# Kernel tuning notes

Hardware: AMD Instinct MI355X
Metric: run time of the kernel (lower is better)

Reference implementation:

```python
import jax, jax.numpy as jnp
import numpy as np

B, L, D = 2, 1024, 2048
E, K = 8, 2
H, HS = 1408, 2816


def setup_inputs() -> dict:
    key = jax.random.key(0)
    ks = jax.random.split(key, 9)
    s = 0.02  # param init scale
    return {
        "x": jax.random.normal(ks[0], (B, L, D), dtype=jnp.float32),
        "gate_w": jax.random.normal(ks[1], (E, D), dtype=jnp.float32) * s,
        "w_gate": jax.random.normal(ks[2], (E, D, H), dtype=jnp.float32) * s,
        "w_up": jax.random.normal(ks[3], (E, D, H), dtype=jnp.float32) * s,
        "w_down": jax.random.normal(ks[4], (E, H, D), dtype=jnp.float32) * s,
        "shgate_w": jax.random.normal(ks[5], (D,), dtype=jnp.float32) * s,
        "shw_gate": jax.random.normal(ks[6], (D, HS), dtype=jnp.float32) * s,
        "shw_up": jax.random.normal(ks[7], (D, HS), dtype=jnp.float32) * s,
        "shw_down": jax.random.normal(ks[8], (HS, D), dtype=jnp.float32) * s,
    }


def reference(x, gate_w, w_gate, w_up, w_down, shgate_w, shw_gate, shw_up, shw_down):
    b, l, d = x.shape
    xf = x.reshape(-1, d)  # [T, D]

    # --- router: softmax over expert logits, top-k, renormalize ---
    logits = jnp.einsum("td,ed->te", xf.astype(jnp.float32), gate_w)
    probs = jax.nn.softmax(logits.astype(jnp.float32), axis=-1)  # [T, E]
    weights, indices = jax.lax.top_k(probs, K)                   # [T, K]
    weights = (weights / weights.sum(-1, keepdims=True)).astype(x.dtype)

    # per-token combine weight for each expert: sum of top-k weights routed to e
    onehot = jax.nn.one_hot(indices, E, dtype=x.dtype)           # [T, K, E]
    combine = jnp.einsum("tk,tke->te", weights, onehot)          # [T, E]

    # --- experts (dense vectorized equivalent of masked gather/scatter loop) ---
    g = jnp.einsum("td,edh->teh", xf, w_gate)
    u = jnp.einsum("td,edh->teh", xf, w_up)
    h = jax.nn.silu(g) * u                                       # [T, E, H]
    # fused down-proj + weighted combine; accumulate in fp32 like the original
    out = jnp.einsum("teh,ehd,te->td", h.astype(jnp.float32),
                     w_down.astype(jnp.float32), combine.astype(jnp.float32))

    # --- shared expert with sigmoid gate ---
    sgate = jax.nn.sigmoid(xf @ shgate_w)[:, None]               # [T, 1]
    sh = (jax.nn.silu(xf @ shw_gate) * (xf @ shw_up)) @ shw_down  # [T, D]
    out = out + (sgate * sh).astype(jnp.float32)

    return out.astype(x.dtype).reshape(b, l, d)
```

## Files before the change

### kernel.cpp

```cpp
#include <hip/hip_runtime.h>
#include <hip/hip_bf16.h>
#include <math.h>

#define T_TOK 2048
#define Dd    2048
#define Ee    8
#define Hh    1408
#define HSs   2816
#define CAP   1024

typedef __attribute__((ext_vector_type(8))) __bf16 bf16x8;
typedef __attribute__((ext_vector_type(4))) __bf16 bf16x4;
typedef __attribute__((ext_vector_type(2))) __bf16 bf16x2;
typedef __attribute__((ext_vector_type(4))) float  f32x4;

#define MFMA(a, b, c) __builtin_amdgcn_mfma_f32_16x16x32_bf16(a, b, c, 0, 0, 0)

__device__ __forceinline__ void async_copy16(const __bf16* g, __bf16* l) {
    __builtin_amdgcn_global_load_lds(
        (const __attribute__((address_space(1))) unsigned int*)g,
        (__attribute__((address_space(3))) unsigned int*)l, 16, 0, 0);
}

__global__ void init_cnt(int* __restrict__ cnt) {
    if (threadIdx.x < Ee) cnt[threadIdx.x] = 0;
}

__global__ __launch_bounds__(256) void router_kernel(
    const float* __restrict__ x, const float* __restrict__ gate_w,
    const float* __restrict__ shgate_w,
    int* __restrict__ cnt, int* __restrict__ ptok, int* __restrict__ pslot,
    float* __restrict__ pw, float* __restrict__ sgate)
{
    const int t = blockIdx.x;
    const int tid = threadIdx.x;
    const float* xt = x + (size_t)t * Dd;

    float acc[Ee];
#pragma unroll
    for (int e = 0; e < Ee; e++) acc[e] = 0.f;
    float accs = 0.f;

    for (int d = tid; d < Dd; d += 256) {
        float xv = xt[d];
#pragma unroll
        for (int e = 0; e < Ee; e++) acc[e] += xv * gate_w[e * Dd + d];
        accs += xv * shgate_w[d];
    }

    __shared__ float red[Ee + 1][256];
#pragma unroll
    for (int e = 0; e < Ee; e++) red[e][tid] = acc[e];
    red[Ee][tid] = accs;
    __syncthreads();

    for (int s = 128; s > 0; s >>= 1) {
        if (tid < s) {
#pragma unroll
            for (int e = 0; e <= Ee; e++) red[e][tid] += red[e][tid + s];
        }
        __syncthreads();
    }

    if (tid == 0) {
        float l0 = -1e30f, l1 = -1e30f;
        int i0 = 0, i1 = 0;
#pragma unroll
        for (int e = 0; e < Ee; e++) {
            float v = red[e][0];
            if (v > l0) { l1 = l0; i1 = i0; l0 = v; i0 = e; }
            else if (v > l1) { l1 = v; i1 = e; }
        }
        float w0 = 1.f / (1.f + expf(l1 - l0));
        float w1 = 1.f - w0;

        int p0 = atomicAdd(&cnt[i0], 1);
        if (p0 < CAP) {
            ptok[i0 * CAP + p0] = t; pslot[i0 * CAP + p0] = 2 * t;
            pw[i0 * CAP + p0] = w0;
        }
        int p1 = atomicAdd(&cnt[i1], 1);
        if (p1 < CAP) {
            ptok[i1 * CAP + p1] = t; pslot[i1 * CAP + p1] = 2 * t + 1;
            pw[i1 * CAP + p1] = w1;
        }
        sgate[t] = 1.f / (1.f + expf(-red[Ee][0]));
    }
}

__global__ __launch_bounds__(256) void cvt_x(const float* __restrict__ src,
                                             __bf16* __restrict__ dst)
{
    int i = blockIdx.x * 256 + threadIdx.x;
    float4 v = ((const float4*)src)[i];
    bf16x4 o = { (__bf16)v.x, (__bf16)v.y, (__bf16)v.z, (__bf16)v.w };
    ((bf16x4*)dst)[i] = o;
}

__global__ __launch_bounds__(256) void transpose_cvt(
    const float* __restrict__ src, __bf16* __restrict__ dst, int R, int C)
{
    src += (size_t)blockIdx.z * R * C;
    dst += (size_t)blockIdx.z * R * C;
    __shared__ float tile[64][65];
    const int tid = threadIdx.x, tx = tid & 63, ty = tid >> 6;
    const int c0 = blockIdx.x * 64, r0 = blockIdx.y * 64;
#pragma unroll
    for (int j = 0; j < 16; j++) {
        int r = j * 4 + ty;
        tile[r][tx] = src[(size_t)(r0 + r) * C + c0 + tx];
    }
    __syncthreads();
    const int rp = (tid & 31) * 2;
    const int cg = tid >> 5;
#pragma unroll
    for (int j = 0; j < 8; j++) {
        int c = j * 8 + cg;
        bf16x2 v = { (__bf16)tile[rp][c], (__bf16)tile[rp + 1][c] };
        *(bf16x2*)&dst[(size_t)(c0 + c) * R + r0 + rp] = v;
    }
}

__global__ __launch_bounds__(256, 3) void gateup_all(
    const __bf16* __restrict__ xb,
    const __bf16* __restrict__ wgT, const __bf16* __restrict__ wuT,
    const __bf16* __restrict__ shwgT, const __bf16* __restrict__ shwuT,
    const int* __restrict__ cnt, const int* __restrict__ ptok,
    __bf16* __restrict__ hq, __bf16* __restrict__ shh)
{
    const int bx = blockIdx.x;
    const int tid = threadIdx.x, lane = tid & 63, wave = tid >> 6;
    const int wr = wave >> 1, wc = wave & 1;
    const int lm = lane & 15, lq = lane >> 4;

    bool sh;
    int m0, h0, n, e = 0;
    const __bf16 *bg_mat, *bu_mat;
    if (bx < 1408) {
        sh = false;
        int mtg = bx / 22, ht = bx - mtg * 22;
        e = mtg >> 3; m0 = (mtg & 7) * 128; h0 = ht * 64;
        n = cnt[e]; if (n > CAP) n = CAP;
        if (m0 >= n) return;
        bg_mat = wgT + (size_t)e * Hh * Dd;
        bu_mat = wuT + (size_t)e * Hh * Dd;
    } else {
        sh = true;
        int s = bx - 1408;
        int mt = s / 44, ht = s - mt * 44;
        m0 = mt * 128; h0 = ht * 64; n = T_TOK;
        bg_mat = shwgT; bu_mat = shwuT;
    }

    __shared__ __align__(16) __bf16 stage[8192];
    __shared__ int tok_s[128];

    if (tid < 128) {
        int i = m0 + tid;
        if (sh) tok_s[tid] = i;
        else { int ic = i < n ? i : n - 1; tok_s[tid] = ptok[e * CAP + ic]; }
    }
    __syncthreads();

    const __bf16* pa0 = xb + (size_t)tok_s[wave * 16 + lm] * Dd + lq * 8;
    const __bf16* pa1 = xb + (size_t)tok_s[64 + wave * 16 + lm] * Dd + lq * 8;
    const __bf16* pbg = bg_mat + (size_t)(h0 + wave * 16 + lm) * Dd + lq * 8;
    const __bf16* pbu = bu_mat + (size_t)(h0 + wave * 16 + lm) * Dd + lq * 8;
    __bf16* la0 = stage + wave * 512 + lane * 8;
    __bf16* la1 = stage + (4 + wave) * 512 + lane * 8;
    __bf16* lbg = stage + 4096 + wave * 512 + lane * 8;
    __bf16* lbu = stage + 6144 + wave * 512 + lane * 8;

    f32x4 acc[4][4] = {};

    for (int k0 = 0; k0 < Dd; k0 += 32) {
        async_copy16(pa0, la0); async_copy16(pa1, la1);
        async_copy16(pbg, lbg); async_copy16(pbu, lbu);
        pa0 += 32; pa1 += 32; pbg += 32; pbu += 32;
        __syncthreads();
        bf16x8 af[4], bfr[4];
        const __bf16* bbase = stage + (wc ? 6144 : 4096);
#pragma unroll
        for (int i = 0; i < 4; i++)
            af[i] = *(const bf16x8*)(stage + (wr * 4 + i) * 512 + lane * 8);
#pragma unroll
        for (int j = 0; j < 4; j++)
            bfr[j] = *(const bf16x8*)(bbase + j * 512 + lane * 8);
#pragma unroll
        for (int i = 0; i < 4; i++)
#pragma unroll
            for (int j = 0; j < 4; j++)
                acc[i][j] = MFMA(af[i], bfr[j], acc[i][j]);
        __syncthreads();
    }

    if (wc == 1) {
#pragma unroll
        for (int i = 0; i < 4; i++)
#pragma unroll
            for (int j = 0; j < 4; j++) {
                bf16x4 uv;
#pragma unroll
                for (int r = 0; r < 4; r++) uv[r] = (__bf16)acc[i][j][r];
                *(bf16x4*)(stage + ((wr * 4 + i) * 4 + j) * 256 + lane * 4) = uv;
            }
    }
    __syncthreads();
    if (wc == 0) {
#pragma unroll
        for (int i = 0; i < 4; i++)
#pragma unroll
            for (int j = 0; j < 4; j++) {
                bf16x4 uv = *(const bf16x4*)(stage + ((wr * 4 + i) * 4 + j) * 256 + lane * 4);
                int col = h0 + j * 16 + lm;
#pragma unroll
                for (int r = 0; r < 4; r++) {
                    int grow = m0 + wr * 64 + i * 16 + lq * 4 + r;
                    if (!sh && grow >= n) continue;
                    float g = acc[i][j][r], u = (float)uv[r];
                    float hv = g / (1.f + __expf(-g)) * u;
                    if (sh) shh[(size_t)grow * HSs + col] = (__bf16)hv;
                    else    hq[((size_t)e * CAP + grow) * Hh + col] = (__bf16)hv;
                }
            }
    }
}

__global__ __launch_bounds__(256, 3) void down_all(
    const __bf16* __restrict__ hq, const __bf16* __restrict__ wdT,
    const __bf16* __restrict__ shh, const __bf16* __restrict__ shwdT,
    const int* __restrict__ cnt, const int* __restrict__ pslot,
    const float* __restrict__ pw, const float* __restrict__ sgate,
    float* __restrict__ eo, float* __restrict__ out)
{
    const int bx = blockIdx.x;
    const int tid = threadIdx.x, lane = tid & 63, wave = tid >> 6;
    const int wr = wave >> 1, wc = wave & 1;
    const int lm = lane & 15, lq = lane >> 4;

    bool sh;
    int m0, n0, n, e = 0, kdim;
    if (bx < 1024) {
        sh = false;
        e = bx >> 7; m0 = ((bx >> 4) & 7) * 128; n0 = (bx & 15) * 128;
        n = cnt[e]; if (n > CAP) n = CAP;
        if (m0 >= n) return;
        kdim = Hh;
    } else {
        sh = true;
        int s = bx - 1024;
        m0 = (s >> 4) * 128; n0 = (s & 15) * 128; n = T_TOK;
        kdim = HSs;
    }

    __shared__ __align__(16) __bf16 stage[8192];
    __shared__ int   slot_s[128];
    __shared__ float w_s[128];

    if (!sh && tid < 128) {
        int i = m0 + tid; int ic = i < n ? i : n - 1;
        slot_s[tid] = pslot[e * CAP + ic];
        w_s[tid] = (i < n) ? pw[e * CAP + ic] : 0.f;
    }

    int ar0 = m0 + wave * 16 + lm, ar1 = m0 + 64 + wave * 16 + lm;
    const __bf16 *pa0, *pa1, *pb0, *pb1;
    if (sh) {
        pa0 = shh + (size_t)ar0 * HSs + lq * 8;
        pa1 = shh + (size_t)ar1 * HSs + lq * 8;
        pb0 = shwdT + (size_t)(n0 + wave * 16 + lm) * HSs + lq * 8;
        pb1 = shwdT + (size_t)(n0 + 64 + wave * 16 + lm) * HSs + lq * 8;
    } else {
        int a0c = ar0 < n ? ar0 : n - 1;
        int a1c = ar1 < n ? ar1 : n - 1;
        pa0 = hq + ((size_t)e * CAP + a0c) * Hh + lq * 8;
        pa1 = hq + ((size_t)e * CAP + a1c) * Hh + lq * 8;
        pb0 = wdT + ((size_t)e * Dd + n0 + wave * 16 + lm) * Hh + lq * 8;
        pb1 = wdT + ((size_t)e * Dd + n0 + 64 + wave * 16 + lm) * Hh + lq * 8;
    }
    __bf16* la0 = stage + wave * 512 + lane * 8;
    __bf16* la1 = stage + (4 + wave) * 512 + lane * 8;
    __bf16* lb0 = stage + 4096 + wave * 512 + lane * 8;
    __bf16* lb1 = stage + 4096 + (4 + wave) * 512 + lane * 8;

    f32x4 acc[4][4] = {};

    for (int k0 = 0; k0 < kdim; k0 += 32) {
        async_copy16(pa0, la0); async_copy16(pa1, la1);
        async_copy16(pb0, lb0); async_copy16(pb1, lb1);
        pa0 += 32; pa1 += 32; pb0 += 32; pb1 += 32;
        __syncthreads();
        bf16x8 af[4], bfr[4];
#pragma unroll
        for (int i = 0; i < 4; i++)
            af[i] = *(const bf16x8*)(stage + (wr * 4 + i) * 512 + lane * 8);
#pragma unroll
        for (int j = 0; j < 4; j++)
            bfr[j] = *(const bf16x8*)(stage + 4096 + (wc * 4 + j) * 512 + lane * 8);
#pragma unroll
        for (int i = 0; i < 4; i++)
#pragma unroll
            for (int j = 0; j < 4; j++)
                acc[i][j] = MFMA(af[i], bfr[j], acc[i][j]);
        __syncthreads();
    }

#pragma unroll
    for (int i = 0; i < 4; i++)
#pragma unroll
        for (int r = 0; r < 4; r++) {
            int rloc = wr * 64 + i * 16 + lq * 4 + r;
            if (sh) {
                int t = m0 + rloc;
                float sg = sgate[t];
#pragma unroll
                for (int j = 0; j < 4; j++)
                    out[(size_t)t * Dd + n0 + (wc * 4 + j) * 16 + lm] = sg * acc[i][j][r];
            } else if (m0 + rloc < n) {
                int   slot = slot_s[rloc];
                float w    = w_s[rloc];
#pragma unroll
                for (int j = 0; j < 4; j++)
                    eo[(size_t)slot * Dd + n0 + (wc * 4 + j) * 16 + lm] = w * acc[i][j][r];
            }
        }
}

__global__ __launch_bounds__(256) void combine_kernel(
    const float* __restrict__ eo, float* __restrict__ out)
{
    int i4 = blockIdx.x * 256 + threadIdx.x;
    int t = i4 >> 9;
    int c = i4 & 511;
    float4 o = ((const float4*)out)[i4];
    float4 a = ((const float4*)(eo + (size_t)(2 * t) * Dd))[c];
    float4 b = ((const float4*)(eo + (size_t)(2 * t + 1) * Dd))[c];
    o.x += a.x + b.x; o.y += a.y + b.y; o.z += a.z + b.z; o.w += a.w + b.w;
    ((float4*)out)[i4] = o;
}

extern "C" void kernel_launch(void* const* d_in, const int* in_sizes, int n_in,
                              void* d_out, int out_size, void* d_ws, size_t ws_size,
                              hipStream_t stream) {
    const float* x        = (const float*)d_in[0];
    const float* gate_w   = (const float*)d_in[1];
    const float* w_gate   = (const float*)d_in[2];
    const float* w_up     = (const float*)d_in[3];
    const float* w_down   = (const float*)d_in[4];
    const float* shgate_w = (const float*)d_in[5];
    const float* shw_gate = (const float*)d_in[6];
    const float* shw_up   = (const float*)d_in[7];
    const float* shw_down = (const float*)d_in[8];
    float* out = (float*)d_out;

    char* ws = (char*)d_ws;
    size_t off = 0;
    auto alloc = [&](size_t bytes) { char* p = ws + off; off = (off + bytes + 255) & ~(size_t)255; return p; };
    int*    cnt    = (int*)   alloc(Ee * 4);
    int*    ptok   = (int*)   alloc(Ee * CAP * 4);
    int*    pslot  = (int*)   alloc(Ee * CAP * 4);
    float*  pw     = (float*) alloc(Ee * CAP * 4);
    float*  sgate  = (float*) alloc(T_TOK * 4);
    __bf16* xb     = (__bf16*)alloc((size_t)T_TOK * Dd * 2);
    __bf16* wgT    = (__bf16*)alloc((size_t)Ee * Hh * Dd * 2);
    __bf16* wuT    = (__bf16*)alloc((size_t)Ee * Hh * Dd * 2);
    __bf16* wdT    = (__bf16*)alloc((size_t)Ee * Dd * Hh * 2);
    __bf16* shwgT  = (__bf16*)alloc((size_t)HSs * Dd * 2);
    __bf16* shwuT  = (__bf16*)alloc((size_t)HSs * Dd * 2);
    __bf16* shwdT  = (__bf16*)alloc((size_t)Dd * HSs * 2);
    __bf16* hq     = (__bf16*)alloc((size_t)Ee * CAP * Hh * 2);
    __bf16* shh    = (__bf16*)alloc((size_t)T_TOK * HSs * 2);
    float*  eo     = (float*) alloc((size_t)T_TOK * 2 * Dd * 4);

    dim3 b256(256);

    init_cnt<<<dim3(1), dim3(64), 0, stream>>>(cnt);
    router_kernel<<<dim3(T_TOK), b256, 0, stream>>>(
        x, gate_w, shgate_w, cnt, ptok, pslot, pw, sgate);
    cvt_x<<<dim3(T_TOK * Dd / 4 / 256), b256, 0, stream>>>(x, xb);
    transpose_cvt<<<dim3(Hh / 64, Dd / 64, Ee), b256, 0, stream>>>(w_gate, wgT, Dd, Hh);
    transpose_cvt<<<dim3(Hh / 64, Dd / 64, Ee), b256, 0, stream>>>(w_up, wuT, Dd, Hh);
    transpose_cvt<<<dim3(Dd / 64, Hh / 64, Ee), b256, 0, stream>>>(w_down, wdT, Hh, Dd);
    transpose_cvt<<<dim3(HSs / 64, Dd / 64, 1), b256, 0, stream>>>(shw_gate, shwgT, Dd, HSs);
    transpose_cvt<<<dim3(HSs / 64, Dd / 64, 1), b256, 0, stream>>>(shw_up, shwuT, Dd, HSs);
    transpose_cvt<<<dim3(Dd / 64, HSs / 64, 1), b256, 0, stream>>>(shw_down, shwdT, HSs, Dd);

    gateup_all<<<dim3(1408 + 704), b256, 0, stream>>>(
        xb, wgT, wuT, shwgT, shwuT, cnt, ptok, hq, shh);
    down_all<<<dim3(1024 + 256), b256, 0, stream>>>(
        hq, wdT, shh, shwdT, cnt, pslot, pw, sgate, eo, out);
    combine_kernel<<<dim3(T_TOK * Dd / 4 / 256), b256, 0, stream>>>(eo, out);
}
```

Measured before the change: 811.7 us.

## Enlarge GEMM tiles in gate/up and down kernels for more reuse per load

The gate/up kernel now computes a 128x128 output tile, with each wave holding both gate and up accumulators. This removes the LDS round-trip used to pair them, and each A fragment now feeds two MFMAs. The down kernel widens its N tile from 128 to 256 columns, so each wave holds 4x8 accumulators. Both kernels halve their grid size and launch bounds drop from 3 to 2 blocks per SIMD. The larger tiles are meant to cut redundant global/LDS traffic per FLOP, in exchange for more registers and LDS, lower occupancy and fewer blocks to balance load.

```diff
diff --git a/kernel.cpp b/kernel.cpp
--- a/kernel.cpp
+++ b/kernel.cpp
@@ -121,7 +121,7 @@
     }
 }
 
-__global__ __launch_bounds__(256, 3) void gateup_all(
+__global__ __launch_bounds__(256, 2) void gateup_all(
     const __bf16* __restrict__ xb,
     const __bf16* __restrict__ wgT, const __bf16* __restrict__ wuT,
     const __bf16* __restrict__ shwgT, const __bf16* __restrict__ shwuT,
@@ -136,23 +136,22 @@
     bool sh;
     int m0, h0, n, e = 0;
     const __bf16 *bg_mat, *bu_mat;
-    if (bx < 1408) {
+    if (bx < 704) {
         sh = false;
-        int mtg = bx / 22, ht = bx - mtg * 22;
-        e = mtg >> 3; m0 = (mtg & 7) * 128; h0 = ht * 64;
+        e = bx / 88; int rem = bx - e * 88;
+        h0 = (rem >> 3) * 128; m0 = (rem & 7) * 128;
         n = cnt[e]; if (n > CAP) n = CAP;
         if (m0 >= n) return;
         bg_mat = wgT + (size_t)e * Hh * Dd;
         bu_mat = wuT + (size_t)e * Hh * Dd;
     } else {
         sh = true;
-        int s = bx - 1408;
-        int mt = s / 44, ht = s - mt * 44;
-        m0 = mt * 128; h0 = ht * 64; n = T_TOK;
+        int s = bx - 704;
+        h0 = (s >> 4) * 128; m0 = (s & 15) * 128; n = T_TOK;
         bg_mat = shwgT; bu_mat = shwuT;
     }
 
-    __shared__ __align__(16) __bf16 stage[8192];
+    __shared__ __align__(16) __bf16 stage[12288];
     __shared__ int tok_s[128];
 
     if (tid < 128) {
@@ -164,69 +163,62 @@
 
     const __bf16* pa0 = xb + (size_t)tok_s[wave * 16 + lm] * Dd + lq * 8;
     const __bf16* pa1 = xb + (size_t)tok_s[64 + wave * 16 + lm] * Dd + lq * 8;
-    const __bf16* pbg = bg_mat + (size_t)(h0 + wave * 16 + lm) * Dd + lq * 8;
-    const __bf16* pbu = bu_mat + (size_t)(h0 + wave * 16 + lm) * Dd + lq * 8;
+    const __bf16* pg0 = bg_mat + (size_t)(h0 + wave * 16 + lm) * Dd + lq * 8;
+    const __bf16* pg1 = bg_mat + (size_t)(h0 + 64 + wave * 16 + lm) * Dd + lq * 8;
+    const __bf16* pu0 = bu_mat + (size_t)(h0 + wave * 16 + lm) * Dd + lq * 8;
+    const __bf16* pu1 = bu_mat + (size_t)(h0 + 64 + wave * 16 + lm) * Dd + lq * 8;
     __bf16* la0 = stage + wave * 512 + lane * 8;
     __bf16* la1 = stage + (4 + wave) * 512 + lane * 8;
-    __bf16* lbg = stage + 4096 + wave * 512 + lane * 8;
-    __bf16* lbu = stage + 6144 + wave * 512 + lane * 8;
-
-    f32x4 acc[4][4] = {};
+    __bf16* lg0 = stage + 4096 + wave * 512 + lane * 8;
+    __bf16* lg1 = stage + 4096 + (4 + wave) * 512 + lane * 8;
+    __bf16* lu0 = stage + 8192 + wave * 512 + lane * 8;
+    __bf16* lu1 = stage + 8192 + (4 + wave) * 512 + lane * 8;
+
+    f32x4 accg[4][4] = {}, accu[4][4] = {};
 
     for (int k0 = 0; k0 < Dd; k0 += 32) {
         async_copy16(pa0, la0); async_copy16(pa1, la1);
-        async_copy16(pbg, lbg); async_copy16(pbu, lbu);
-        pa0 += 32; pa1 += 32; pbg += 32; pbu += 32;
-        __syncthreads();
-        bf16x8 af[4], bfr[4];
-        const __bf16* bbase = stage + (wc ? 6144 : 4096);
+        async_copy16(pg0, lg0); async_copy16(pg1, lg1);
+        async_copy16(pu0, lu0); async_copy16(pu1, lu1);
+        pa0 += 32; pa1 += 32; pg0 += 32; pg1 += 32; pu0 += 32; pu1 += 32;
+        __syncthreads();
+        bf16x8 af[4], gf[4], uf[4];
 #pragma unroll
         for (int i = 0; i < 4; i++)
             af[i] = *(const bf16x8*)(stage + (wr * 4 + i) * 512 + lane * 8);
 #pragma unroll
-        for (int j = 0; j < 4; j++)
-            bfr[j] = *(const bf16x8*)(bbase + j * 512 + lane * 8);
+        for (int j = 0; j < 4; j++) {
+            gf[j] = *(const bf16x8*)(stage + 4096 + (wc * 4 + j) * 512 + lane * 8);
+            uf[j] = *(const bf16x8*)(stage + 8192 + (wc * 4 + j) * 512 + lane * 8);
+        }
 #pragma unroll
         for (int i = 0; i < 4; i++)
 #pragma unroll
-            for (int j = 0; j < 4; j++)
-                acc[i][j] = MFMA(af[i], bfr[j], acc[i][j]);
-        __syncthreads();
-    }
-
-    if (wc == 1) {
-#pragma unroll
-        for (int i = 0; i < 4; i++)
-#pragma unroll
             for (int j = 0; j < 4; j++) {
-                bf16x4 uv;
-#pragma unroll
-                for (int r = 0; r < 4; r++) uv[r] = (__bf16)acc[i][j][r];
-                *(bf16x4*)(stage + ((wr * 4 + i) * 4 + j) * 256 + lane * 4) = uv;
+                accg[i][j] = MFMA(af[i], gf[j], accg[i][j]);
+                accu[i][j] = MFMA(af[i], uf[j], accu[i][j]);
             }
-    }
-    __syncthreads();
-    if (wc == 0) {
-#pragma unroll
-        for (int i = 0; i < 4; i++)
+        __syncthreads();
+    }
+
+#pragma unroll
+    for (int i = 0; i < 4; i++)
+#pragma unroll
+        for (int r = 0; r < 4; r++) {
+            int grow = m0 + wr * 64 + i * 16 + lq * 4 + r;
+            if (!sh && grow >= n) continue;
 #pragma unroll
             for (int j = 0; j < 4; j++) {
-                bf16x4 uv = *(const bf16x4*)(stage + ((wr * 4 + i) * 4 + j) * 256 + lane * 4);
-                int col = h0 + j * 16 + lm;
-#pragma unroll
-                for (int r = 0; r < 4; r++) {
-                    int grow = m0 + wr * 64 + i * 16 + lq * 4 + r;
-                    if (!sh && grow >= n) continue;
-                    float g = acc[i][j][r], u = (float)uv[r];
-                    float hv = g / (1.f + __expf(-g)) * u;
-                    if (sh) shh[(size_t)grow * HSs + col] = (__bf16)hv;
-                    else    hq[((size_t)e * CAP + grow) * Hh + col] = (__bf16)hv;
-                }
+                int col = h0 + wc * 64 + j * 16 + lm;
+                float g = accg[i][j][r], u = accu[i][j][r];
+                float hv = g / (1.f + __expf(-g)) * u;
+                if (sh) shh[(size_t)grow * HSs + col] = (__bf16)hv;
+                else    hq[((size_t)e * CAP + grow) * Hh + col] = (__bf16)hv;
             }
-    }
-}
-
-__global__ __launch_bounds__(256, 3) void down_all(
+        }
+}
+
+__global__ __launch_bounds__(256, 2) void down_all(
     const __bf16* __restrict__ hq, const __bf16* __restrict__ wdT,
     const __bf16* __restrict__ shh, const __bf16* __restrict__ shwdT,
     const int* __restrict__ cnt, const int* __restrict__ pslot,
@@ -240,20 +232,21 @@
 
     bool sh;
     int m0, n0, n, e = 0, kdim;
-    if (bx < 1024) {
+    if (bx < 512) {
         sh = false;
-        e = bx >> 7; m0 = ((bx >> 4) & 7) * 128; n0 = (bx & 15) * 128;
+        e = bx >> 6; int rem = bx & 63;
+        n0 = (rem >> 3) * 256; m0 = (rem & 7) * 128;
         n = cnt[e]; if (n > CAP) n = CAP;
         if (m0 >= n) return;
         kdim = Hh;
     } else {
         sh = true;
-        int s = bx - 1024;
-        m0 = (s >> 4) * 128; n0 = (s & 15) * 128; n = T_TOK;
+        int s = bx - 512;
+        n0 = (s >> 4) * 256; m0 = (s & 15) * 128; n = T_TOK;
         kdim = HSs;
     }
 
-    __shared__ __align__(16) __bf16 stage[8192];
+    __shared__ __align__(16) __bf16 stage[12288];
     __shared__ int   slot_s[128];
     __shared__ float w_s[128];
 
@@ -264,12 +257,14 @@
     }
 
     int ar0 = m0 + wave * 16 + lm, ar1 = m0 + 64 + wave * 16 + lm;
-    const __bf16 *pa0, *pa1, *pb0, *pb1;
+    const __bf16 *pa0, *pa1, *pb0, *pb1, *pb2, *pb3;
     if (sh) {
         pa0 = shh + (size_t)ar0 * HSs + lq * 8;
         pa1 = shh + (size_t)ar1 * HSs + lq * 8;
         pb0 = shwdT + (size_t)(n0 + wave * 16 + lm) * HSs + lq * 8;
         pb1 = shwdT + (size_t)(n0 + 64 + wave * 16 + lm) * HSs + lq * 8;
+        pb2 = shwdT + (size_t)(n0 + 128 + wave * 16 + lm) * HSs + lq * 8;
+        pb3 = shwdT + (size_t)(n0 + 192 + wave * 16 + lm) * HSs + lq * 8;
     } else {
         int a0c = ar0 < n ? ar0 : n - 1;
         int a1c = ar1 < n ? ar1 : n - 1;
@@ -277,30 +272,35 @@
         pa1 = hq + ((size_t)e * CAP + a1c) * Hh + lq * 8;
         pb0 = wdT + ((size_t)e * Dd + n0 + wave * 16 + lm) * Hh + lq * 8;
         pb1 = wdT + ((size_t)e * Dd + n0 + 64 + wave * 16 + lm) * Hh + lq * 8;
+        pb2 = wdT + ((size_t)e * Dd + n0 + 128 + wave * 16 + lm) * Hh + lq * 8;
+        pb3 = wdT + ((size_t)e * Dd + n0 + 192 + wave * 16 + lm) * Hh + lq * 8;
     }
     __bf16* la0 = stage + wave * 512 + lane * 8;
     __bf16* la1 = stage + (4 + wave) * 512 + lane * 8;
     __bf16* lb0 = stage + 4096 + wave * 512 + lane * 8;
     __bf16* lb1 = stage + 4096 + (4 + wave) * 512 + lane * 8;
-
-    f32x4 acc[4][4] = {};
+    __bf16* lb2 = stage + 4096 + (8 + wave) * 512 + lane * 8;
+    __bf16* lb3 = stage + 4096 + (12 + wave) * 512 + lane * 8;
+
+    f32x4 acc[4][8] = {};
 
     for (int k0 = 0; k0 < kdim; k0 += 32) {
         async_copy16(pa0, la0); async_copy16(pa1, la1);
         async_copy16(pb0, lb0); async_copy16(pb1, lb1);
-        pa0 += 32; pa1 += 32; pb0 += 32; pb1 += 32;
-        __syncthreads();
-        bf16x8 af[4], bfr[4];
+        async_copy16(pb2, lb2); async_copy16(pb3, lb3);
+        pa0 += 32; pa1 += 32; pb0 += 32; pb1 += 32; pb2 += 32; pb3 += 32;
+        __syncthreads();
+        bf16x8 af[4], bfr[8];
 #pragma unroll
         for (int i = 0; i < 4; i++)
             af[i] = *(const bf16x8*)(stage + (wr * 4 + i) * 512 + lane * 8);
 #pragma unroll
-        for (int j = 0; j < 4; j++)
-            bfr[j] = *(const bf16x8*)(stage + 4096 + (wc * 4 + j) * 512 + lane * 8);
+        for (int j = 0; j < 8; j++)
+            bfr[j] = *(const bf16x8*)(stage + 4096 + (wc * 8 + j) * 512 + lane * 8);
 #pragma unroll
         for (int i = 0; i < 4; i++)
 #pragma unroll
-            for (int j = 0; j < 4; j++)
+            for (int j = 0; j < 8; j++)
                 acc[i][j] = MFMA(af[i], bfr[j], acc[i][j]);
         __syncthreads();
     }
@@ -314,14 +314,14 @@
                 int t = m0 + rloc;
                 float sg = sgate[t];
 #pragma unroll
-                for (int j = 0; j < 4; j++)
-                    out[(size_t)t * Dd + n0 + (wc * 4 + j) * 16 + lm] = sg * acc[i][j][r];
+                for (int j = 0; j < 8; j++)
+                    out[(size_t)t * Dd + n0 + wc * 128 + j * 16 + lm] = sg * acc[i][j][r];
             } else if (m0 + rloc < n) {
                 int   slot = slot_s[rloc];
                 float w    = w_s[rloc];
 #pragma unroll
-                for (int j = 0; j < 4; j++)
-                    eo[(size_t)slot * Dd + n0 + (wc * 4 + j) * 16 + lm] = w * acc[i][j][r];
+                for (int j = 0; j < 8; j++)
+                    eo[(size_t)slot * Dd + n0 + wc * 128 + j * 16 + lm] = w * acc[i][j][r];
             }
         }
 }
@@ -385,9 +385,9 @@
     transpose_cvt<<<dim3(HSs / 64, Dd / 64, 1), b256, 0, stream>>>(shw_up, shwuT, Dd, HSs);
     transpose_cvt<<<dim3(Dd / 64, HSs / 64, 1), b256, 0, stream>>>(shw_down, shwdT, HSs, Dd);
 
-    gateup_all<<<dim3(1408 + 704), b256, 0, stream>>>(
+    gateup_all<<<dim3(704 + 352), b256, 0, stream>>>(
         xb, wgT, wuT, shwgT, shwuT, cnt, ptok, hq, shh);
-    down_all<<<dim3(1024 + 256), b256, 0, stream>>>(
+    down_all<<<dim3(512 + 128), b256, 0, stream>>>(
         hq, wdT, shh, shwdT, cnt, pslot, pw, sgate, eo, out);
     combine_kernel<<<dim3(T_TOK * Dd / 4 / 256), b256, 0, stream>>>(eo, out);
 }
```

Result: slower. 881.2 us (+8.6%).
